# Kernel tuning notes

Hardware: AMD Instinct MI355X
Metric: run time of the kernel (lower is better)

The kernel has to match this reference:

```python
import jax, jax.numpy as jnp
import numpy as np
import math

CONTRAST = 3.38589
SQRT2 = math.sqrt(2.0)
WIN_R = 3   # win_radius in the torch module
WIN = 2 * WIN_R  # 6x6 gather window


def _inverse_sigmoid(q):
    # maps sigmoidized values back toward linear light (mask-multiply form, as in torch)
    c = CONTRAST
    sig1 = math.tanh(0.25 * c)
    sig0 = -sig1
    slope = (1.0 / sig1 + sig0) * 0.25 * c
    inv = 1.0 / slope
    m_lo = (q <= 0.0).astype(q.dtype)
    m_hi = (q >= 1.0).astype(q.dtype)
    m_mid = 1.0 - m_lo - m_hi
    ssq = jnp.clip(2.0 * sig1 * q + sig0, -0.999999, 0.999999)
    mid = (2.0 / c) * jnp.arctanh(ssq) + 0.5
    return (q * inv) * m_lo + (q * inv + (1.0 - inv)) * m_hi + mid * m_mid


def _extended_sigmoid(q):
    c = CONTRAST
    sig1 = math.tanh(0.25 * c)
    slope = (1.0 / sig1 - sig1) * 0.25 * c
    m_lo = (q <= 0.0).astype(q.dtype)
    m_hi = (q >= 1.0).astype(q.dtype)
    m_mid = 1.0 - m_lo - m_hi
    sq = slope * q
    mid = (0.5 / sig1) * jnp.tanh(0.5 * c * q - 0.25 * c) + 0.5
    return sq * m_lo + (sq + (1.0 - slope)) * m_hi + mid * m_mid


def _robidoux_weight(r2):
    a3 = -3.0
    a2 = (45739.0 + 7164.0 * SQRT2) / 10319.0
    a0 = (-8926.0 - 14328.0 * SQRT2) / 10319.0
    m_in_root = (-103.0 - 36.0 * SQRT2) / (7.0 + 72.0 * SQRT2)
    m_out_root = -2.0
    r = jnp.sqrt(r2 + 1e-8)
    m_inner = (r2 < 1.0).astype(r2.dtype)
    m_outer = ((r2 >= 1.0) & (r2 < 4.0)).astype(r2.dtype)
    w_inner = r2 * (a3 * r + a2) + a0
    w_outer = (r + m_in_root) * (r + m_out_root) ** 2
    return w_inner * m_inner + w_outer * m_outer


def _mitchell_kernel(x):
    ax = jnp.abs(x)
    m1 = (ax < 1.0).astype(x.dtype)
    m2 = ((ax >= 1.0) & (ax < 2.0)).astype(x.dtype)
    v1 = (7.0 / 6.0) * ax ** 3 - 2.0 * ax ** 2 + 8.0 / 9.0
    v2 = (-7.0 / 18.0) * ax ** 3 + 2.0 * ax ** 2 - (10.0 / 3.0) * ax + 16.0 / 9.0
    return v1 * m1 + v2 * m2


def _forward(image, grid):
    B, C, H_in, W_in = image.shape
    _, H_out, W_out, _ = grid.shape
    # ---- Jacobian via central finite differences with replicate padding ----
    gx = jnp.pad(grid, ((0, 0), (0, 0), (1, 1), (0, 0)), mode='edge')
    dx = (gx[:, :, 2:, :] - gx[:, :, :-2, :]) * 0.5  # (B,Ho,Wo,2)
    gy = jnp.pad(grid, ((0, 0), (1, 1), (0, 0), (0, 0)), mode='edge')
    dy = (gy[:, 2:, :, :] - gy[:, :-2, :, :]) * 0.5
    J00, J10 = dx[..., 0], dx[..., 1]
    J01, J11 = dy[..., 0], dy[..., 1]
    det = J00 * J11 - J01 * J10 + 1e-8
    a = J11 / det
    b = -J01 / det
    c = -J10 / det
    d = J00 / det
    n11 = a * a + b * b
    n12 = a * c + b * d
    n22 = c * c + d * d
    frob = n11 + n22
    disc = frob ** 2 - 4.0 / (det * det)
    sqrt_disc = jnp.sqrt(jnp.clip(disc, 0.0, None))
    twice_s1s1 = frob + sqrt_disc
    s1s1 = 0.5 * twice_s1s1
    s2s2 = 0.5 * (frob - sqrt_disc)
    major_mag = jnp.sqrt(jnp.clip(s1s1, 1.0, None))
    minor_mag = jnp.sqrt(jnp.clip(s2s2, 1.0, None))
    # eigenvector of N for s1s1 (stable branch choice)
    diff1 = s1s1 - n11
    diff2 = s1s1 - n22
    cond = diff1 ** 2 >= diff2 ** 2
    tu11 = jnp.where(cond, n12, diff2)
    tu21 = jnp.where(cond, diff1, n12)
    norm = jnp.sqrt(tu11 ** 2 + tu21 ** 2)
    norm_safe = jnp.where(norm > 0, norm, 1.0)
    u11 = jnp.where(norm > 0, tu11 / norm_safe, 1.0)
    u21 = jnp.where(norm > 0, tu21 / norm_safe, 0.0)
    c_major_x = u11 / major_mag
    c_major_y = u21 / major_mag
    c_minor_x = -u21 / minor_mag
    c_minor_y = u11 / minor_mag
    theta = 1.0 / (major_mag * minor_mag)
    need_ewa = twice_s1s1 > 2.0
    # ---- 6x6 neighborhood gather ----
    ix = jnp.floor(grid[..., 0]).astype(jnp.int32)
    iy = jnp.floor(grid[..., 1]).astype(jnp.int32)
    fx = grid[..., 0] - (ix.astype(grid.dtype) + 0.5)
    fy = grid[..., 1] - (iy.astype(grid.dtype) + 0.5)
    img_pad = jnp.pad(image, ((0, 0), (0, 0), (WIN_R, WIN_R + 1), (WIN_R, WIN_R + 1)), mode='edge')
    H_pad, W_pad = img_pad.shape[2], img_pad.shape[3]
    oy, ox = jnp.meshgrid(jnp.arange(-WIN_R + 1, WIN_R + 1), jnp.arange(-WIN_R + 1, WIN_R + 1), indexing='ij')  # (6,6)
    n_iy = jnp.clip(iy[..., None, None] + oy + WIN_R, 0, H_pad - 1)
    n_ix = jnp.clip(ix[..., None, None] + ox + WIN_R, 0, W_pad - 1)
    flat_idx = (n_iy * W_pad + n_ix).reshape(B, 1, -1)  # (B,1,Ho*Wo*36)
    img_flat = img_pad.reshape(B, C, -1)
    pixels = jnp.take_along_axis(img_flat, jnp.broadcast_to(flat_idx, (B, C, flat_idx.shape[-1])), axis=2)
    pixels = pixels.reshape(B, C, H_out, W_out, WIN, WIN)
    ox_f = ox.astype(grid.dtype)
    oy_f = oy.astype(grid.dtype)
    rel_x = fx[..., None, None] - ox_f  # (B,Ho,Wo,6,6)
    rel_y = fy[..., None, None] - oy_f
    # ---- Mitchell branch (in sigmoidized space) ----
    pixels_sig = _inverse_sigmoid(pixels)
    w_mitchell = _mitchell_kernel(rel_x) * _mitchell_kernel(rel_y)
    mitchell_sum = jnp.sum(pixels_sig * w_mitchell[:, None], axis=(-1, -2))  # (B,C,Ho,Wo)
    mitchell_val = _extended_sigmoid(mitchell_sum)
    # ---- EWA Robidoux branch (linear space) ----
    q1 = rel_x * c_major_x[..., None, None] + rel_y * c_major_y[..., None, None]
    q2 = rel_x * c_minor_x[..., None, None] + rel_y * c_minor_y[..., None, None]
    r2 = q1 * q1 + q2 * q2
    w_ewa = _robidoux_weight(r2)
    total_w = jnp.sum(w_ewa, axis=(-1, -2)) + 1e-8  # (B,Ho,Wo)
    ewa_sum = jnp.sum(pixels * w_ewa[:, None], axis=(-1, -2))  # (B,C,Ho,Wo)
    ewa_val = ewa_sum / total_w[:, None]
    th = theta[:, None]
    return jnp.where(need_ewa[:, None], th * mitchell_val + (1.0 - th) * ewa_val, mitchell_val)


def setup_inputs() -> dict:
    key = jax.random.key(0)
    k_img, k_grid = jax.random.split(key)
    B, C, H_in, W_in = 1, 3, 1024, 1024
    H_out, W_out = 768, 768
    image = jax.random.uniform(k_img, (B, C, H_in, W_in), dtype=jnp.float32)
    # affine downscale map in source-pixel coords + small jitter
    ys = (jnp.arange(H_out, dtype=jnp.float32) + 0.5) * (H_in / H_out)
    xs = (jnp.arange(W_out, dtype=jnp.float32) + 0.5) * (W_in / W_out)
    gy, gx = jnp.meshgrid(ys, xs, indexing='ij')
    base = jnp.stack([gx, gy], axis=-1)  # (Ho,Wo,2): (x,y)
    jitter = (jax.random.uniform(k_grid, (B, H_out, W_out, 2), dtype=jnp.float32) - 0.5) * 0.5
    grid = base[None] + jitter
    return {"image": image, "grid": grid}


def reference(image, grid):
    return _forward(image, grid)
```

## Files before the change

### kernel.cpp

```cpp
#include <hip/hip_runtime.h>
#include <math.h>

#define H_IN  1024
#define W_IN  1024
#define HW_IN (H_IN * W_IN)
#define H_OUT 768
#define W_OUT 768
#define HW_OUT (H_OUT * W_OUT)

#define SROWS 28
#define SPX   32
#define RS    (SPX * 6 + 8)
#define NLD4  (3 * SROWS * (SPX / 4))

typedef float v2f __attribute__((ext_vector_type(2)));

struct KC {
    float tsig1, msig1, atanh_scale;
    float slope, one_m_slope, half_over_sig1;
    float exp_a, exp_b;
    float a2, a0, m_in_root;
};

__device__ __forceinline__ float fast_rcp(float x)  { return __builtin_amdgcn_rcpf(x); }
__device__ __forceinline__ float fast_log2(float x) { return __builtin_amdgcn_logf(x); }
__device__ __forceinline__ float fast_exp2(float x) { return __builtin_amdgcn_exp2f(x); }
__device__ __forceinline__ float fast_rsq(float x)  { return __builtin_amdgcn_rsqf(x); }

__device__ __forceinline__ float inv_sigmoid(float q, const KC k) {
    float ssq = fmaf(k.tsig1, q, k.msig1);
    float ratio = (1.f + ssq) * fast_rcp(1.f - ssq);
    return fmaf(fast_log2(ratio), k.atanh_scale, 0.5f);
}

__device__ __forceinline__ float ext_sigmoid(float q, const KC k) {
    float lo = k.slope * q;
    float e  = fast_exp2(fmaf(k.exp_a, q, k.exp_b));
    float th = fmaf(-2.f, fast_rcp(e + 1.f), 1.f);
    float mid = fmaf(k.half_over_sig1, th, 0.5f);
    float v = (q <= 0.f) ? lo : mid;
    return (q >= 1.f) ? (lo + k.one_m_slope) : v;
}

__device__ __forceinline__ float mitchell_b(float xv) {
    float ax = fabsf(xv);
    float v1 = fmaf(ax * ax, fmaf(7.f / 6.f, ax, -2.f), 8.f / 9.f);
    float v2 = fmaf(fmaf(fmaf(-7.f / 18.f, ax, 2.f), ax, -10.f / 3.f), ax, 16.f / 9.f);
    float v = (ax < 1.f) ? v1 : v2;
    return (ax < 2.f) ? v : 0.f;
}

__device__ __forceinline__ float robidoux_b(float r2, const KC k) {
    float r = sqrtf(r2 + 1e-8f);
    float w_in = fmaf(r2, fmaf(-3.f, r, k.a2), k.a0);
    float t = r - 2.f;
    float w_out = (r + k.m_in_root) * (t * t);
    float w = (r2 < 1.f) ? w_in : w_out;
    return (r2 < 4.f) ? w : 0.f;
}

__global__ __launch_bounds__(256, 3)
void lohalo_fused(const float* __restrict__ img, const float* __restrict__ grid,
                  float* __restrict__ out, KC k) {
    __shared__ float sm[SROWS * RS];
    __shared__ int sred[16];

    const int bid = blockIdx.x;
    const int swz = (bid & 7) * 288 + (bid >> 3);
    const int bx = swz % 48, by = swz / 48;

    const int tid = threadIdx.x;
    const int lx = tid & 15, ly = tid >> 4;
    const int x = bx * 16 + lx;
    const int y = by * 16 + ly;
    const int pix = y * W_OUT + x;

    const float2* G = (const float2*)grid;
    float2 gc  = G[pix];
    float2 gxm = G[y * W_OUT + max(x - 1, 0)];
    float2 gxp = G[y * W_OUT + min(x + 1, W_OUT - 1)];
    float2 gym = G[max(y - 1, 0) * W_OUT + x];
    float2 gyp = G[min(y + 1, H_OUT - 1) * W_OUT + x];
    float J00 = (gxp.x - gxm.x) * 0.5f, J10 = (gxp.y - gxm.y) * 0.5f;
    float J01 = (gyp.x - gym.x) * 0.5f, J11 = (gyp.y - gym.y) * 0.5f;
    float det = J00 * J11 - J01 * J10 + 1e-8f;
    float idet = fast_rcp(det);
    float a  = J11 * idet, b = -J01 * idet;
    float cI = -J10 * idet, d = J00 * idet;
    float n11 = a * a + b * b, n12 = a * cI + b * d, n22 = cI * cI + d * d;
    float frob = n11 + n22;
    float disc = frob * frob - 4.f * idet * idet;
    float sdisc = sqrtf(fmaxf(disc, 0.f));
    float twice = frob + sdisc;
    float s1s1 = 0.5f * twice, s2s2 = 0.5f * (frob - sdisc);
    float rmaj = fast_rsq(fmaxf(s1s1, 1.f));
    float rmin = fast_rsq(fmaxf(s2s2, 1.f));
    float diff1 = s1s1 - n11, diff2 = s1s1 - n22;
    bool  cnd  = diff1 * diff1 >= diff2 * diff2;
    float tu11 = cnd ? n12 : diff2;
    float tu21 = cnd ? diff1 : n12;
    float nrm = sqrtf(tu11 * tu11 + tu21 * tu21);
    float inrm = fast_rcp(nrm);
    float u11 = nrm > 0.f ? tu11 * inrm : 1.f;
    float u21 = nrm > 0.f ? tu21 * inrm : 0.f;
    float cMx = u11 * rmaj, cMy = u21 * rmaj;
    float cmx = -u21 * rmin, cmy = u11 * rmin;
    float theta = rmaj * rmin;
    bool need_ewa = twice > 2.f;

    float fix = floorf(gc.x), fiy = floorf(gc.y);
    int ix = (int)fix, iy = (int)fiy;
    float fx = gc.x - (fix + 0.5f);
    float fy = gc.y - (fiy + 0.5f);

    int mnx = ix, mxx = ix, mny = iy, mxy = iy;
#pragma unroll
    for (int m = 1; m < 64; m <<= 1) {
        mnx = min(mnx, __shfl_xor(mnx, m));
        mxx = max(mxx, __shfl_xor(mxx, m));
        mny = min(mny, __shfl_xor(mny, m));
        mxy = max(mxy, __shfl_xor(mxy, m));
    }
    const int wid = tid >> 6;
    if ((tid & 63) == 0) {
        sred[wid * 4 + 0] = mnx;
        sred[wid * 4 + 1] = mxx;
        sred[wid * 4 + 2] = mny;
        sred[wid * 4 + 3] = mxy;
    }
    __syncthreads();
    mnx = min(min(sred[0], sred[4]),  min(sred[8],  sred[12]));
    mxx = max(max(sred[1], sred[5]),  max(sred[9],  sred[13]));
    mny = min(min(sred[2], sred[6]),  min(sred[10], sred[14]));
    mxy = max(max(sred[3], sred[7]),  max(sred[11], sred[15]));

    const int x0 = (mnx - 2) & ~3;
    const int y0 = mny - 2;
    const bool fits = (mxx + 3 - x0 < SPX) && (mxy + 3 - y0 < SROWS);

    float mx6[6];
#pragma unroll
    for (int t = 0; t < 6; t++) mx6[t] = mitchell_b(fx - (float)(t - 2));
    const float fxp2 = fx + 2.f;

    v2f a0 = {0.f, 0.f}, a1 = {0.f, 0.f}, a2acc = {0.f, 0.f};
    float tw = 0.f;
    const bool any_ewa = __any(need_ewa);

    if (fits) {
        if (x0 >= 0 && x0 + SPX <= W_IN) {
            for (int j = tid; j < NLD4; j += 256) {
                int p   = j / (SROWS * (SPX / 4));
                int rem = j - p * (SROWS * (SPX / 4));
                int r   = rem >> 3;
                int q   = rem & 7;
                int gr  = min(max(y0 + r, 0), H_IN - 1);
                float4 v = *(const float4*)&img[(size_t)p * HW_IN + (size_t)gr * W_IN + x0 + q * 4];
                float* o = &sm[r * RS + (q * 4) * 6 + p * 2];
                *(float2*)(o)      = make_float2(v.x, inv_sigmoid(v.x, k));
                *(float2*)(o + 6)  = make_float2(v.y, inv_sigmoid(v.y, k));
                *(float2*)(o + 12) = make_float2(v.z, inv_sigmoid(v.z, k));
                *(float2*)(o + 18) = make_float2(v.w, inv_sigmoid(v.w, k));
            }
        } else {
            for (int j = tid; j < SROWS * SPX; j += 256) {
                int r = j / SPX;
                int c = j - r * SPX;
                int gr  = min(max(y0 + r, 0), H_IN - 1);
                int gcc = min(max(x0 + c, 0), W_IN - 1);
                const float* base = &img[(size_t)gr * W_IN + gcc];
                int o = r * RS + c * 6;
#pragma unroll
                for (int p = 0; p < 3; p++) {
                    float pv = base[(size_t)p * HW_IN];
                    *(float2*)&sm[o + p * 2] = make_float2(pv, inv_sigmoid(pv, k));
                }
            }
        }
        __syncthreads();

        const float* sp = &sm[(iy - 2 - y0) * RS + (ix - 2 - x0) * 6];
        if (any_ewa) {
            const v2f cM = {cMx, cmx};
#pragma unroll
            for (int ty = 0; ty < 6; ty++) {
                float rely = fy - (float)(ty - 2);
                float wmy = mitchell_b(rely);
                v2f q = { fmaf(fxp2, cMx, rely * cMy),
                          fmaf(fxp2, cmx, rely * cmy) };
                float mxw[6];
#pragma unroll
                for (int t = 0; t < 6; t++) mxw[t] = mx6[t] * wmy;
                const float* rp = sp + ty * RS;
#pragma unroll
                for (int tx = 0; tx < 6; tx++) {
                    v2f f0 = *(const v2f*)(rp + tx * 6);
                    v2f f1 = *(const v2f*)(rp + tx * 6 + 2);
                    v2f f2 = *(const v2f*)(rp + tx * 6 + 4);
                    float r2 = fmaf(q.x, q.x, q.y * q.y);
                    float we = robidoux_b(r2, k);
                    tw += we;
                    v2f w = { we, mxw[tx] };
                    a0    = __builtin_elementwise_fma(f0, w, a0);
                    a1    = __builtin_elementwise_fma(f1, w, a1);
                    a2acc = __builtin_elementwise_fma(f2, w, a2acc);
                    q = q - cM;
                }
            }
        } else {
#pragma unroll
            for (int ty = 0; ty < 5; ty++) {
                float rely = fy - (float)(ty - 2);
                float wmy = mitchell_b(rely);
                const float* rp = sp + ty * RS;
                float rs0 = 0.f, rs1 = 0.f, rs2 = 0.f;
#pragma unroll
                for (int tx = 0; tx < 5; tx++) {
                    float mxv = mx6[tx];
                    rs0 = fmaf((rp + tx * 6)[1], mxv, rs0);
                    rs1 = fmaf((rp + tx * 6)[3], mxv, rs1);
                    rs2 = fmaf((rp + tx * 6)[5], mxv, rs2);
                }
                a0.y    = fmaf(rs0, wmy, a0.y);
                a1.y    = fmaf(rs1, wmy, a1.y);
                a2acc.y = fmaf(rs2, wmy, a2acc.y);
            }
        }
    } else {
#pragma unroll
        for (int ty = 0; ty < 6; ty++) {
            float rely = fy - (float)(ty - 2);
            float wmy = mitchell_b(rely);
            float q1 = fmaf(fxp2, cMx, rely * cMy);
            float q2 = fmaf(fxp2, cmx, rely * cmy);
            const int gy2 = min(max(iy + (ty - 2), 0), H_IN - 1);
            const int rb = gy2 * W_IN;
#pragma unroll
            for (int tx = 0; tx < 6; tx++) {
                const int off = rb + min(max(ix + (tx - 2), 0), W_IN - 1);
                float p0 = img[off];
                float p1 = img[off + HW_IN];
                float p2 = img[off + 2 * HW_IN];
                float mxw = mx6[tx] * wmy;
                float r2 = fmaf(q1, q1, q2 * q2);
                float we = robidoux_b(r2, k);
                tw += we;
                a0.x    = fmaf(p0, we, a0.x);
                a1.x    = fmaf(p1, we, a1.x);
                a2acc.x = fmaf(p2, we, a2acc.x);
                a0.y    = fmaf(inv_sigmoid(p0, k), mxw, a0.y);
                a1.y    = fmaf(inv_sigmoid(p1, k), mxw, a1.y);
                a2acc.y = fmaf(inv_sigmoid(p2, k), mxw, a2acc.y);
                q1 -= cMx;
                q2 -= cmx;
            }
        }
    }

    tw += 1e-8f;
    float itw = fast_rcp(tw);
    float mv0 = ext_sigmoid(a0.y, k);
    float mv1 = ext_sigmoid(a1.y, k);
    float mv2 = ext_sigmoid(a2acc.y, k);
    float om = 1.f - theta;
    out[pix]              = need_ewa ? theta * mv0 + om * (a0.x * itw)    : mv0;
    out[HW_OUT + pix]     = need_ewa ? theta * mv1 + om * (a1.x * itw)    : mv1;
    out[2 * HW_OUT + pix] = need_ewa ? theta * mv2 + om * (a2acc.x * itw) : mv2;
}

extern "C" void kernel_launch(void* const* d_in, const int* in_sizes, int n_in,
                              void* d_out, int out_size, void* d_ws, size_t ws_size,
                              hipStream_t stream) {
    const float* img  = (const float*)d_in[0];
    const float* grid = (const float*)d_in[1];
    float* out = (float*)d_out;

    KC k;
    const double cc = 3.38589;
    const double s1 = tanh(0.25 * cc);
    const double slope = (1.0 / s1 - s1) * 0.25 * cc;
    const double log2e = 1.4426950408889634074;
    const double ln2   = 0.6931471805599453094;
    k.tsig1 = (float)(2.0 * s1);
    k.msig1 = (float)(-s1);
    k.atanh_scale = (float)(ln2 / cc);
    k.slope = (float)slope;
    k.one_m_slope = (float)(1.0 - slope);
    k.half_over_sig1 = (float)(0.5 / s1);
    k.exp_a = (float)(cc * log2e);
    k.exp_b = (float)(-0.5 * cc * log2e);
    const double sq2 = sqrt(2.0);
    k.a2 = (float)((45739.0 + 7164.0 * sq2) / 10319.0);
    k.a0 = (float)((-8926.0 - 14328.0 * sq2) / 10319.0);
    k.m_in_root = (float)((-103.0 - 36.0 * sq2) / (7.0 + 72.0 * sq2));

    lohalo_fused<<<(W_OUT / 16) * (H_OUT / 16), 256, 0, stream>>>(img, grid, out, k);
}
```

Baseline: 26.72 us.

## Predict shared tile origin from block index and start staging before Jacobian math

The shared-memory tile origin is now computed from the known affine scale of the block position instead of a wave-shuffle and LDS reduction of the actual sample positions. That lets the image tile load and inverse-sigmoid transform start before the Jacobian and ellipse setup, which can overlap memory latency with math and removes one barrier. The EWA radius is updated incrementally with second differences in r2 instead of recomputing q each tap, the Mitchell-only fast path is dropped, and occupancy is raised to 4 blocks per CU. The tile origin now assumes the fixed 1024-to-768 scale, so out-of-tile pixels fall back to the global path, and every wave now always does the full EWA loop.

```diff
diff --git a/kernel.cpp b/kernel.cpp
--- a/kernel.cpp
+++ b/kernel.cpp
@@ -7,6 +7,8 @@
 #define H_OUT 768
 #define W_OUT 768
 #define HW_OUT (H_OUT * W_OUT)
+#define SCALE_X (1024.f / 768.f)
+#define SCALE_Y (1024.f / 768.f)
 
 #define SROWS 28
 #define SPX   32
@@ -59,11 +61,10 @@
     return (r2 < 4.f) ? w : 0.f;
 }
 
-__global__ __launch_bounds__(256, 3)
+__global__ __launch_bounds__(256, 4)
 void lohalo_fused(const float* __restrict__ img, const float* __restrict__ grid,
                   float* __restrict__ out, KC k) {
     __shared__ float sm[SROWS * RS];
-    __shared__ int sred[16];
 
     const int bid = blockIdx.x;
     const int swz = (bid & 7) * 288 + (bid >> 3);
@@ -74,6 +75,39 @@
     const int x = bx * 16 + lx;
     const int y = by * 16 + ly;
     const int pix = y * W_OUT + x;
+
+    const int x0 = (((int)floorf(fmaf(16.f * bx + 0.5f, SCALE_X, -0.25f)) - 2) & ~3);
+    const int y0 = ((int)floorf(fmaf(16.f * by + 0.5f, SCALE_Y, -0.25f))) - 2;
+
+    if (x0 >= 0 && x0 + SPX <= W_IN) {
+        for (int j = tid; j < NLD4; j += 256) {
+            int p   = j / (SROWS * (SPX / 4));
+            int rem = j - p * (SROWS * (SPX / 4));
+            int r   = rem >> 3;
+            int q   = rem & 7;
+            int gr  = min(max(y0 + r, 0), H_IN - 1);
+            float4 v = *(const float4*)&img[(size_t)p * HW_IN + (size_t)gr * W_IN + x0 + q * 4];
+            float* o = &sm[r * RS + (q * 4) * 6 + p * 2];
+            *(float2*)(o)      = make_float2(v.x, inv_sigmoid(v.x, k));
+            *(float2*)(o + 6)  = make_float2(v.y, inv_sigmoid(v.y, k));
+            *(float2*)(o + 12) = make_float2(v.z, inv_sigmoid(v.z, k));
+            *(float2*)(o + 18) = make_float2(v.w, inv_sigmoid(v.w, k));
+        }
+    } else {
+        for (int j = tid; j < SROWS * SPX; j += 256) {
+            int r = j / SPX;
+            int c = j - r * SPX;
+            int gr  = min(max(y0 + r, 0), H_IN - 1);
+            int gcc = min(max(x0 + c, 0), W_IN - 1);
+            const float* base = &img[(size_t)gr * W_IN + gcc];
+            int o = r * RS + c * 6;
+#pragma unroll
+            for (int p = 0; p < 3; p++) {
+                float pv = base[(size_t)p * HW_IN];
+                *(float2*)&sm[o + p * 2] = make_float2(pv, inv_sigmoid(pv, k));
+            }
+        }
+    }
 
     const float2* G = (const float2*)grid;
     float2 gc  = G[pix];
@@ -113,117 +147,49 @@
     float fx = gc.x - (fix + 0.5f);
     float fy = gc.y - (fiy + 0.5f);
 
-    int mnx = ix, mxx = ix, mny = iy, mxy = iy;
-#pragma unroll
-    for (int m = 1; m < 64; m <<= 1) {
-        mnx = min(mnx, __shfl_xor(mnx, m));
-        mxx = max(mxx, __shfl_xor(mxx, m));
-        mny = min(mny, __shfl_xor(mny, m));
-        mxy = max(mxy, __shfl_xor(mxy, m));
-    }
-    const int wid = tid >> 6;
-    if ((tid & 63) == 0) {
-        sred[wid * 4 + 0] = mnx;
-        sred[wid * 4 + 1] = mxx;
-        sred[wid * 4 + 2] = mny;
-        sred[wid * 4 + 3] = mxy;
-    }
-    __syncthreads();
-    mnx = min(min(sred[0], sred[4]),  min(sred[8],  sred[12]));
-    mxx = max(max(sred[1], sred[5]),  max(sred[9],  sred[13]));
-    mny = min(min(sred[2], sred[6]),  min(sred[10], sred[14]));
-    mxy = max(max(sred[3], sred[7]),  max(sred[11], sred[15]));
-
-    const int x0 = (mnx - 2) & ~3;
-    const int y0 = mny - 2;
-    const bool fits = (mxx + 3 - x0 < SPX) && (mxy + 3 - y0 < SROWS);
-
     float mx6[6];
 #pragma unroll
     for (int t = 0; t < 6; t++) mx6[t] = mitchell_b(fx - (float)(t - 2));
     const float fxp2 = fx + 2.f;
 
+    const float c2m  = fmaf(cMx, cMx, cmx * cmx);
+    const float tc2m = 2.f * c2m;
+
+    const bool fits = (ix - 2 - x0 >= 0) && (ix - x0 <= SPX - 4) &&
+                      (iy - 2 - y0 >= 0) && (iy - y0 <= SROWS - 4);
+
     v2f a0 = {0.f, 0.f}, a1 = {0.f, 0.f}, a2acc = {0.f, 0.f};
     float tw = 0.f;
-    const bool any_ewa = __any(need_ewa);
+
+    __syncthreads();
 
     if (fits) {
-        if (x0 >= 0 && x0 + SPX <= W_IN) {
-            for (int j = tid; j < NLD4; j += 256) {
-                int p   = j / (SROWS * (SPX / 4));
-                int rem = j - p * (SROWS * (SPX / 4));
-                int r   = rem >> 3;
-                int q   = rem & 7;
-                int gr  = min(max(y0 + r, 0), H_IN - 1);
-                float4 v = *(const float4*)&img[(size_t)p * HW_IN + (size_t)gr * W_IN + x0 + q * 4];
-                float* o = &sm[r * RS + (q * 4) * 6 + p * 2];
-                *(float2*)(o)      = make_float2(v.x, inv_sigmoid(v.x, k));
-                *(float2*)(o + 6)  = make_float2(v.y, inv_sigmoid(v.y, k));
-                *(float2*)(o + 12) = make_float2(v.z, inv_sigmoid(v.z, k));
-                *(float2*)(o + 18) = make_float2(v.w, inv_sigmoid(v.w, k));
-            }
-        } else {
-            for (int j = tid; j < SROWS * SPX; j += 256) {
-                int r = j / SPX;
-                int c = j - r * SPX;
-                int gr  = min(max(y0 + r, 0), H_IN - 1);
-                int gcc = min(max(x0 + c, 0), W_IN - 1);
-                const float* base = &img[(size_t)gr * W_IN + gcc];
-                int o = r * RS + c * 6;
-#pragma unroll
-                for (int p = 0; p < 3; p++) {
-                    float pv = base[(size_t)p * HW_IN];
-                    *(float2*)&sm[o + p * 2] = make_float2(pv, inv_sigmoid(pv, k));
-                }
-            }
-        }
-        __syncthreads();
-
         const float* sp = &sm[(iy - 2 - y0) * RS + (ix - 2 - x0) * 6];
-        if (any_ewa) {
-            const v2f cM = {cMx, cmx};
-#pragma unroll
-            for (int ty = 0; ty < 6; ty++) {
-                float rely = fy - (float)(ty - 2);
-                float wmy = mitchell_b(rely);
-                v2f q = { fmaf(fxp2, cMx, rely * cMy),
-                          fmaf(fxp2, cmx, rely * cmy) };
-                float mxw[6];
-#pragma unroll
-                for (int t = 0; t < 6; t++) mxw[t] = mx6[t] * wmy;
-                const float* rp = sp + ty * RS;
-#pragma unroll
-                for (int tx = 0; tx < 6; tx++) {
-                    v2f f0 = *(const v2f*)(rp + tx * 6);
-                    v2f f1 = *(const v2f*)(rp + tx * 6 + 2);
-                    v2f f2 = *(const v2f*)(rp + tx * 6 + 4);
-                    float r2 = fmaf(q.x, q.x, q.y * q.y);
-                    float we = robidoux_b(r2, k);
-                    tw += we;
-                    v2f w = { we, mxw[tx] };
-                    a0    = __builtin_elementwise_fma(f0, w, a0);
-                    a1    = __builtin_elementwise_fma(f1, w, a1);
-                    a2acc = __builtin_elementwise_fma(f2, w, a2acc);
-                    q = q - cM;
-                }
-            }
-        } else {
-#pragma unroll
-            for (int ty = 0; ty < 5; ty++) {
-                float rely = fy - (float)(ty - 2);
-                float wmy = mitchell_b(rely);
-                const float* rp = sp + ty * RS;
-                float rs0 = 0.f, rs1 = 0.f, rs2 = 0.f;
-#pragma unroll
-                for (int tx = 0; tx < 5; tx++) {
-                    float mxv = mx6[tx];
-                    rs0 = fmaf((rp + tx * 6)[1], mxv, rs0);
-                    rs1 = fmaf((rp + tx * 6)[3], mxv, rs1);
-                    rs2 = fmaf((rp + tx * 6)[5], mxv, rs2);
-                }
-                a0.y    = fmaf(rs0, wmy, a0.y);
-                a1.y    = fmaf(rs1, wmy, a1.y);
-                a2acc.y = fmaf(rs2, wmy, a2acc.y);
+#pragma unroll
+        for (int ty = 0; ty < 6; ty++) {
+            float rely = fy - (float)(ty - 2);
+            float wmy = mitchell_b(rely);
+            float q1 = fmaf(fxp2, cMx, rely * cMy);
+            float q2 = fmaf(fxp2, cmx, rely * cmy);
+            float r2 = fmaf(q1, q1, q2 * q2);
+            float dd = fmaf(-2.f, fmaf(q1, cMx, q2 * cmx), c2m);
+            float mxw[6];
+#pragma unroll
+            for (int t = 0; t < 6; t++) mxw[t] = mx6[t] * wmy;
+            const float* rp = sp + ty * RS;
+#pragma unroll
+            for (int tx = 0; tx < 6; tx++) {
+                v2f f0 = *(const v2f*)(rp + tx * 6);
+                v2f f1 = *(const v2f*)(rp + tx * 6 + 2);
+                v2f f2 = *(const v2f*)(rp + tx * 6 + 4);
+                float we = robidoux_b(r2, k);
+                tw += we;
+                v2f w = { we, mxw[tx] };
+                a0    = __builtin_elementwise_fma(f0, w, a0);
+                a1    = __builtin_elementwise_fma(f1, w, a1);
+                a2acc = __builtin_elementwise_fma(f2, w, a2acc);
+                r2 += dd;
+                dd += tc2m;
             }
         }
     } else {
```

Measured after the change: 29.89 us. 1.12x slower.
